# Performance work log

Measured on AMD Instinct MI355X. Metric: run time of the kernel, lower is better.

Reference implementation:

```python
import jax, jax.numpy as jnp
import numpy as np

DIM = 512
NUM_HEADS = 8
HEAD_DIM = DIM // NUM_HEADS
SCALE = HEAD_DIM ** -0.5


def setup_inputs() -> dict:
    key = jax.random.key(0)
    kx, kqw, kqb, kpw, kpb = jax.random.split(key, 5)
    B, N = 2, 4096
    x = jax.random.normal(kx, (B, N, DIM), dtype=jnp.float32)
    # nn.Linear weights stored as [out, in]; init ~ U(-1/sqrt(in), 1/sqrt(in))
    bound = 1.0 / np.sqrt(DIM)
    qkv_w = jax.random.uniform(kqw, (3 * DIM, DIM), minval=-bound, maxval=bound, dtype=jnp.float32)
    qkv_b = jax.random.uniform(kqb, (3 * DIM,), minval=-bound, maxval=bound, dtype=jnp.float32)
    proj_w = jax.random.uniform(kpw, (DIM, DIM), minval=-bound, maxval=bound, dtype=jnp.float32)
    proj_b = jax.random.uniform(kpb, (DIM,), minval=-bound, maxval=bound, dtype=jnp.float32)
    return {"x": x, "qkv_w": qkv_w, "qkv_b": qkv_b, "proj_w": proj_w, "proj_b": proj_b}


def reference(x, qkv_w, qkv_b, proj_w, proj_b):
    B, N, C = x.shape
    # qkv: [B, N, 3C] -> [3, B, H, N, Dh]
    qkv = x @ qkv_w.T + qkv_b
    qkv = qkv.reshape(B, N, 3, NUM_HEADS, HEAD_DIM).transpose(2, 0, 3, 1, 4)
    q, k, v = qkv[0], qkv[1], qkv[2]
    # scores: [B, H, N, N] (materialized, matching the original math)
    attn = jnp.einsum("bhqd,bhkd->bhqk", q, k) * SCALE
    attn = jax.nn.softmax(attn, axis=-1)
    out = jnp.einsum("bhqk,bhkd->bhqd", attn, v)  # [B, H, N, Dh]
    out = out.transpose(0, 2, 1, 3).reshape(B, N, C)
    return out @ proj_w.T + proj_b
```

## Files before the change

kernel.cpp:

```cpp
#include <hip/hip_runtime.h>
#include <stdint.h>
#include <stddef.h>

typedef __attribute__((ext_vector_type(8))) short short8;
typedef __attribute__((ext_vector_type(4))) float f32x4;

#define MFMA16(a, b, c) __builtin_amdgcn_mfma_f32_16x16x32_bf16((a), (b), (c), 0, 0, 0)

__device__ __forceinline__ float b2f(short x) {
    unsigned u = ((unsigned)(unsigned short)x) << 16;
    float f; __builtin_memcpy(&f, &u, 4); return f;
}
__device__ __forceinline__ short f2b(float f) {
    unsigned u; __builtin_memcpy(&u, &f, 4);
    u = (u + 0x7FFFu + ((u >> 16) & 1u)) >> 16;
    return (short)u;
}
__device__ __forceinline__ unsigned pack2(float a, float b) {
    unsigned ua, ub; __builtin_memcpy(&ua, &a, 4); __builtin_memcpy(&ub, &b, 4);
    return __builtin_amdgcn_perm(ub + 0x8000u, ua + 0x8000u, 0x07060302u);
}
__device__ __forceinline__ short8 load8f(const float* p) {
    const float4 f0 = *(const float4*)p;
    const float4 f1 = *(const float4*)(p + 4);
    short8 r;
    r[0]=f2b(f0.x); r[1]=f2b(f0.y); r[2]=f2b(f0.z); r[3]=f2b(f0.w);
    r[4]=f2b(f1.x); r[5]=f2b(f1.y); r[6]=f2b(f1.z); r[7]=f2b(f1.w);
    return r;
}

__global__ __launch_bounds__(256) void cvt3(
    const float* __restrict__ s0, short* __restrict__ d0, int n0,
    const float* __restrict__ s1, short* __restrict__ d1, int n1,
    const float* __restrict__ s2, short* __restrict__ d2, int n2)
{
    int i = blockIdx.x * 256 + threadIdx.x;
    if (i < n0) { *(short8*)(d0 + (size_t)i * 8) = load8f(s0 + (size_t)i * 8); return; }
    i -= n0;
    if (i < n1) { *(short8*)(d1 + (size_t)i * 8) = load8f(s1 + (size_t)i * 8); return; }
    i -= n1;
    if (i < n2) { *(short8*)(d2 + (size_t)i * 8) = load8f(s2 + (size_t)i * 8); }
}

__global__ __launch_bounds__(256) void qkv_qk(
    const short* __restrict__ X, const short* __restrict__ W,
    const float* __restrict__ bias,
    short* __restrict__ Qb, short* __restrict__ Kb)
{
    const int tid  = threadIdx.x;
    const int wv   = tid >> 6;
    const int lane = tid & 63;
    const int l15  = lane & 15;
    const int quad = lane >> 4;
    const int m0   = blockIdx.x * 128 + (wv >> 1) * 64;
    const int sec  = blockIdx.y >> 2;
    const int bis  = blockIdx.y & 3;
    const int nbase = sec * 512 + bis * 128;
    const int j0   = (wv & 1) * 64;

    const f32x4 zero = {0.f, 0.f, 0.f, 0.f};
    f32x4 acc[4][4];
#pragma unroll
    for (int i = 0; i < 4; i++)
#pragma unroll
        for (int j = 0; j < 4; j++) acc[i][j] = zero;

    for (int k0 = 0; k0 < 512; k0 += 32) {
        short8 a[4], b[4];
#pragma unroll
        for (int i = 0; i < 4; i++)
            a[i] = *(const short8*)(X + (size_t)(m0 + i * 16 + l15) * 512 + k0 + quad * 8);
#pragma unroll
        for (int j = 0; j < 4; j++)
            b[j] = *(const short8*)(W + (size_t)(nbase + j0 + j * 16 + l15) * 512 + k0 + quad * 8);
#pragma unroll
        for (int i = 0; i < 4; i++)
#pragma unroll
            for (int j = 0; j < 4; j++)
                acc[i][j] = MFMA16(a[i], b[j], acc[i][j]);
    }

#pragma unroll
    for (int j = 0; j < 4; j++) {
        const int jc = bis * 128 + j0 + j * 16 + l15;
        const float bs = bias[sec * 512 + jc];
        const int hl = jc >> 6, d = jc & 63;
#pragma unroll
        for (int i = 0; i < 4; i++) {
#pragma unroll
            for (int r = 0; r < 4; r++) {
                const int m = m0 + i * 16 + quad * 4 + r;
                const int bb = m >> 12, seq = m & 4095;
                const int bh = bb * 8 + hl;
                const float v = acc[i][j][r] + bs;
                if (sec == 0)
                    Qb[((size_t)bh * 4096 + seq) * 64 + d] = f2b(v * 0.125f);
                else
                    Kb[((size_t)bh * 4096 + seq) * 64 + d] = f2b(v);
            }
        }
    }
}

__global__ __launch_bounds__(256) void qkv_v(
    const short* __restrict__ X, const short* __restrict__ W,
    const float* __restrict__ bias, short* __restrict__ Vb)
{
    __shared__ short sT[128][132];

    const int tid  = threadIdx.x;
    const int wv   = tid >> 6;
    const int lane = tid & 63;
    const int l15  = lane & 15;
    const int quad = lane >> 4;
    const int m0   = blockIdx.x * 128 + (wv >> 1) * 64;
    const int bis  = blockIdx.y;
    const int nbase = 1024 + bis * 128;
    const int j0   = (wv & 1) * 64;

    const f32x4 zero = {0.f, 0.f, 0.f, 0.f};
    f32x4 acc[4][4];
#pragma unroll
    for (int i = 0; i < 4; i++)
#pragma unroll
        for (int j = 0; j < 4; j++) acc[i][j] = zero;

    for (int k0 = 0; k0 < 512; k0 += 32) {
        short8 a[4], b[4];
#pragma unroll
        for (int i = 0; i < 4; i++)
            a[i] = *(const short8*)(X + (size_t)(m0 + i * 16 + l15) * 512 + k0 + quad * 8);
#pragma unroll
        for (int j = 0; j < 4; j++)
            b[j] = *(const short8*)(W + (size_t)(nbase + j0 + j * 16 + l15) * 512 + k0 + quad * 8);
#pragma unroll
        for (int i = 0; i < 4; i++)
#pragma unroll
            for (int j = 0; j < 4; j++)
                acc[i][j] = MFMA16(a[i], b[j], acc[i][j]);
    }

#pragma unroll
    for (int j = 0; j < 4; j++) {
        const int jcl = j0 + j * 16 + l15;
        const float bs = bias[nbase + jcl];
#pragma unroll
        for (int i = 0; i < 4; i++) {
            uint2 w;
            w.x = pack2(acc[i][j][0] + bs, acc[i][j][1] + bs);
            w.y = pack2(acc[i][j][2] + bs, acc[i][j][3] + bs);
            *(uint2*)&sT[jcl][(wv >> 1) * 64 + i * 16 + quad * 4] = w;
        }
    }
    __syncthreads();

    const int jcl = tid >> 1, half = tid & 1;
    const int hl = (bis * 128 + jcl) >> 6;
    const int d  = jcl & 63;
    const int bb = (blockIdx.x * 128) >> 12;
    const int seq0 = ((blockIdx.x * 128) & 4095) + half * 64;
    short* dst = Vb + ((size_t)(bb * 8 + hl) * 64 + d) * 4096 + seq0;
#pragma unroll
    for (int u = 0; u < 8; u++)
        *(short8*)(dst + u * 8) = *(const short8*)&sT[jcl][half * 64 + u * 8];
}

__global__ __launch_bounds__(256) void flash_attn(
    const short* __restrict__ Q, const short* __restrict__ K,
    const short* __restrict__ V, short* __restrict__ PO0,
    short* __restrict__ PO1, float* __restrict__ lbuf, int ktiles)
{
    __shared__ short sK[64][72];
    __shared__ short sV[64][72];
    __shared__ short sP[4][2][16][72];

    const int tid  = threadIdx.x;
    const int wv   = tid >> 6;
    const int lane = tid & 63;
    const int l15  = lane & 15;
    const int quad = lane >> 4;
    const int bh = blockIdx.y;
    const int b = bh >> 3, h = bh & 7;
    const int qw = blockIdx.x * 128 + wv * 32;
    const int ks = blockIdx.z;
    const int key0 = ks * ktiles * 64;

    const short* Qb = Q + (size_t)bh * 4096 * 64;
    const short* Kb = K + (size_t)bh * 4096 * 64;
    const short* Vb = V + (size_t)bh * 64 * 4096;

    const short8 aq00 = *(const short8*)(Qb + (size_t)(qw + l15) * 64 + quad * 8);
    const short8 aq01 = *(const short8*)(Qb + (size_t)(qw + l15) * 64 + 32 + quad * 8);
    const short8 aq10 = *(const short8*)(Qb + (size_t)(qw + 16 + l15) * 64 + quad * 8);
    const short8 aq11 = *(const short8*)(Qb + (size_t)(qw + 16 + l15) * 64 + 32 + quad * 8);

    const f32x4 zero = {0.f, 0.f, 0.f, 0.f};
    f32x4 o0[4], o1[4];
    float l0 = 0.f, l1 = 0.f;
#pragma unroll
    for (int r = 0; r < 4; r++) { o0[r] = zero; o1[r] = zero; }

    int srow[2], scb[2];
#pragma unroll
    for (int i = 0; i < 2; i++) {
        const int c = tid + i * 256;
        srow[i] = c >> 3; scb[i] = (c & 7) * 8;
    }

    short8 pk[2], pv[2];
#pragma unroll
    for (int i = 0; i < 2; i++) {
        pk[i] = *(const short8*)(Kb + (size_t)(key0 + srow[i]) * 64 + scb[i]);
        pv[i] = *(const short8*)(Vb + (size_t)srow[i] * 4096 + key0 + scb[i]);
    }

    for (int kt = 0; kt < ktiles; ++kt) {
        const int k0 = key0 + kt * 64;
        __syncthreads();
#pragma unroll
        for (int i = 0; i < 2; i++) {
            *(short8*)&sK[srow[i]][scb[i]] = pk[i];
            *(short8*)&sV[srow[i]][scb[i]] = pv[i];
        }
        __syncthreads();

        if (kt + 1 < ktiles) {
            const int k0n = k0 + 64;
#pragma unroll
            for (int i = 0; i < 2; i++) {
                pk[i] = *(const short8*)(Kb + (size_t)(k0n + srow[i]) * 64 + scb[i]);
                pv[i] = *(const short8*)(Vb + (size_t)srow[i] * 4096 + k0n + scb[i]);
            }
        }

        f32x4 ST0[4], ST1[4];
#pragma unroll
        for (int c = 0; c < 4; c++) {
            const short8 bk0 = *(const short8*)&sK[c * 16 + l15][quad * 8];
            const short8 bk1 = *(const short8*)&sK[c * 16 + l15][32 + quad * 8];
            ST0[c] = MFMA16(bk1, aq01, MFMA16(bk0, aq00, zero));
            ST1[c] = MFMA16(bk1, aq11, MFMA16(bk0, aq10, zero));
        }

#pragma unroll
        for (int c = 0; c < 4; c++) {
            const float p0 = __expf(ST0[c][0]), p1 = __expf(ST0[c][1]);
            const float p2 = __expf(ST0[c][2]), p3 = __expf(ST0[c][3]);
            l0 += (p0 + p1) + (p2 + p3);
            uint2 w; w.x = pack2(p0, p1); w.y = pack2(p2, p3);
            *(uint2*)&sP[wv][0][l15][c * 16 + quad * 4] = w;
            const float r0 = __expf(ST1[c][0]), r1 = __expf(ST1[c][1]);
            const float r2 = __expf(ST1[c][2]), r3 = __expf(ST1[c][3]);
            l1 += (r0 + r1) + (r2 + r3);
            uint2 v; v.x = pack2(r0, r1); v.y = pack2(r2, r3);
            *(uint2*)&sP[wv][1][l15][c * 16 + quad * 4] = v;
        }
        __threadfence_block();

        const short8 bp00 = *(const short8*)&sP[wv][0][l15][quad * 8];
        const short8 bp01 = *(const short8*)&sP[wv][0][l15][32 + quad * 8];
        const short8 bp10 = *(const short8*)&sP[wv][1][l15][quad * 8];
        const short8 bp11 = *(const short8*)&sP[wv][1][l15][32 + quad * 8];

#pragma unroll
        for (int td = 0; td < 4; td++) {
            const short8 bv0 = *(const short8*)&sV[td * 16 + l15][quad * 8];
            const short8 bv1 = *(const short8*)&sV[td * 16 + l15][32 + quad * 8];
            o0[td] = MFMA16(bv0, bp00, o0[td]);
            o0[td] = MFMA16(bv1, bp01, o0[td]);
            o1[td] = MFMA16(bv0, bp10, o1[td]);
            o1[td] = MFMA16(bv1, bp11, o1[td]);
        }
    }

    l0 += __shfl_xor(l0, 16); l0 += __shfl_xor(l0, 32);
    l1 += __shfl_xor(l1, 16); l1 += __shfl_xor(l1, 32);
    const float inv0 = 1.f / fmaxf(l0, 1e-30f);
    const float inv1 = 1.f / fmaxf(l1, 1e-30f);

    short* PO = (ks == 0) ? PO0 : PO1;
#pragma unroll
    for (int td = 0; td < 4; td++) {
        uint2 w0, w1;
        w0.x = pack2(o0[td][0] * inv0, o0[td][1] * inv0);
        w0.y = pack2(o0[td][2] * inv0, o0[td][3] * inv0);
        w1.x = pack2(o1[td][0] * inv1, o1[td][1] * inv1);
        w1.y = pack2(o1[td][2] * inv1, o1[td][3] * inv1);
        const int col = h * 64 + td * 16 + quad * 4;
        *(uint2*)(PO + ((size_t)b * 4096 + qw + l15) * 512 + col) = w0;
        *(uint2*)(PO + ((size_t)b * 4096 + qw + 16 + l15) * 512 + col) = w1;
    }
    if (lbuf && quad == 0) {
        lbuf[((size_t)ks * 16 + bh) * 4096 + qw + l15] = l0;
        lbuf[((size_t)ks * 16 + bh) * 4096 + qw + 16 + l15] = l1;
    }
}

__global__ __launch_bounds__(256) void combine(
    const short* __restrict__ PO0, short* __restrict__ PO1,
    const float* __restrict__ L)
{
    const int i = blockIdx.x * 256 + threadIdx.x;
    const size_t flat = (size_t)i * 8;
    const int col = (int)(flat & 511);
    const int q   = (int)((flat >> 9) & 4095);
    const int b   = (int)(flat >> 21);
    const int bh  = b * 8 + (col >> 6);
    const float l0 = L[(size_t)bh * 4096 + q];
    const float l1 = L[(size_t)65536 + (size_t)bh * 4096 + q];
    const float inv = 1.f / (l0 + l1);
    const float w0 = l0 * inv, w1 = l1 * inv;
    const short8 a = *(const short8*)(PO0 + flat);
    const short8 c = *(const short8*)(PO1 + flat);
    short8 r;
#pragma unroll
    for (int k = 0; k < 8; k++) r[k] = f2b(w0 * b2f(a[k]) + w1 * b2f(c[k]));
    *(short8*)(PO1 + flat) = r;
}

__global__ __launch_bounds__(256) void proj_piece(
    const short* __restrict__ A, const short* __restrict__ W,
    const float* __restrict__ bias, float* __restrict__ dst, int m_base)
{
    const int tid  = threadIdx.x;
    const int wv   = tid >> 6;
    const int lane = tid & 63;
    const int l15  = lane & 15;
    const int quad = lane >> 4;
    const int m0 = blockIdx.x * 128 + (wv >> 1) * 64;
    const int n0 = blockIdx.y * 128 + (wv & 1) * 64;

    const f32x4 zero = {0.f, 0.f, 0.f, 0.f};
    f32x4 acc[4][4];
#pragma unroll
    for (int i = 0; i < 4; i++)
#pragma unroll
        for (int j = 0; j < 4; j++) acc[i][j] = zero;

    for (int k0 = 0; k0 < 512; k0 += 32) {
        short8 a[4], b[4];
#pragma unroll
        for (int i = 0; i < 4; i++)
            a[i] = *(const short8*)(A + (size_t)(m_base + m0 + i * 16 + l15) * 512 + k0 + quad * 8);
#pragma unroll
        for (int j = 0; j < 4; j++)
            b[j] = *(const short8*)(W + (size_t)(n0 + j * 16 + l15) * 512 + k0 + quad * 8);
#pragma unroll
        for (int i = 0; i < 4; i++)
#pragma unroll
            for (int j = 0; j < 4; j++)
                acc[i][j] = MFMA16(a[i], b[j], acc[i][j]);
    }

#pragma unroll
    for (int j = 0; j < 4; j++) {
        const int n = n0 + j * 16 + l15;
        const float bs = bias[n];
#pragma unroll
        for (int i = 0; i < 4; i++) {
#pragma unroll
            for (int r = 0; r < 4; r++) {
                const int m = m0 + i * 16 + quad * 4 + r;
                dst[(size_t)m * 512 + n] = acc[i][j][r] + bs;
            }
        }
    }
}

extern "C" void kernel_launch(void* const* d_in, const int* in_sizes, int n_in,
                              void* d_out, int out_size, void* d_ws, size_t ws_size,
                              hipStream_t stream)
{
    const float* x      = (const float*)d_in[0];
    const float* qkv_w  = (const float*)d_in[1];
    const float* qkv_b  = (const float*)d_in[2];
    const float* proj_w = (const float*)d_in[3];
    const float* proj_b = (const float*)d_in[4];

    const size_t MB = 1024 * 1024;
    short* xb   = (short*)d_out;
    short* wb   = (short*)d_out + 4 * MB;
    short* attn = (short*)d_out + 4 * MB;
    float* out  = (float*)d_out;

    short* Qf = (short*)d_ws;
    short* Kf = Qf + (size_t)16 * 4096 * 64;
    short* Vf = Kf + (size_t)16 * 4096 * 64;
    float* lbuf = (float*)((char*)d_ws + 24 * MB);
    short* pwb  = (short*)((char*)d_ws + 24 * MB + 512 * 1024);

    cvt3<<<2560, 256, 0, stream>>>(x, xb, 524288, qkv_w, wb, 98304, proj_w, pwb, 32768);
    qkv_qk<<<dim3(64, 8), 256, 0, stream>>>(xb, wb, qkv_b, Qf, Kf);
    qkv_v <<<dim3(64, 4), 256, 0, stream>>>(xb, wb, qkv_b, Vf);
    flash_attn<<<dim3(32, 16, 2), 256, 0, stream>>>(Qf, Kf, Vf, (short*)d_out, attn, lbuf, 32);
    combine<<<2048, 256, 0, stream>>>((const short*)d_out, attn, lbuf);
    proj_piece<<<dim3(32, 4), 256, 0, stream>>>(attn, pwb, proj_b, out, 0);
    proj_piece<<<dim3(32, 4), 256, 0, stream>>>(attn, pwb, proj_b, (float*)d_ws, 4096);
    hipMemcpyAsync((char*)d_out + 8 * MB, d_ws, 8 * MB,
                   hipMemcpyDeviceToDevice, stream);
}
```

Measured before the change: 281.7 us.

## Merge QKV GEMMs, compute softmax row sums via MFMA, use exp2 and hardware bf16 packing

```diff
diff --git a/kernel.cpp b/kernel.cpp
--- a/kernel.cpp
+++ b/kernel.cpp
@@ -1,4 +1,5 @@
 #include <hip/hip_runtime.h>
+#include <hip/hip_bf16.h>
 #include <stdint.h>
 #include <stddef.h>
 
@@ -6,6 +7,8 @@
 typedef __attribute__((ext_vector_type(4))) float f32x4;
 
 #define MFMA16(a, b, c) __builtin_amdgcn_mfma_f32_16x16x32_bf16((a), (b), (c), 0, 0, 0)
+
+#define QSCALE 0.1803368801111204f
 
 __device__ __forceinline__ float b2f(short x) {
     unsigned u = ((unsigned)(unsigned short)x) << 16;
@@ -16,9 +19,9 @@
     u = (u + 0x7FFFu + ((u >> 16) & 1u)) >> 16;
     return (short)u;
 }
-__device__ __forceinline__ unsigned pack2(float a, float b) {
-    unsigned ua, ub; __builtin_memcpy(&ua, &a, 4); __builtin_memcpy(&ub, &b, 4);
-    return __builtin_amdgcn_perm(ub + 0x8000u, ua + 0x8000u, 0x07060302u);
+__device__ __forceinline__ unsigned pkrn(float a, float b) {
+    __hip_bfloat162 h = __float22bfloat162_rn(float2{a, b});
+    unsigned u; __builtin_memcpy(&u, &h, 4); return u;
 }
 __device__ __forceinline__ short8 load8f(const float* p) {
     const float4 f0 = *(const float4*)p;
@@ -42,11 +45,13 @@
     if (i < n2) { *(short8*)(d2 + (size_t)i * 8) = load8f(s2 + (size_t)i * 8); }
 }
 
-__global__ __launch_bounds__(256) void qkv_qk(
+__global__ __launch_bounds__(256) void qkv_gemm(
     const short* __restrict__ X, const short* __restrict__ W,
     const float* __restrict__ bias,
-    short* __restrict__ Qb, short* __restrict__ Kb)
-{
+    short* __restrict__ Qb, short* __restrict__ Kb, short* __restrict__ Vb)
+{
+    __shared__ short sT[128][132];
+
     const int tid  = threadIdx.x;
     const int wv   = tid >> 6;
     const int lane = tid & 63;
@@ -80,89 +85,50 @@
                 acc[i][j] = MFMA16(a[i], b[j], acc[i][j]);
     }
 
-#pragma unroll
-    for (int j = 0; j < 4; j++) {
-        const int jc = bis * 128 + j0 + j * 16 + l15;
-        const float bs = bias[sec * 512 + jc];
-        const int hl = jc >> 6, d = jc & 63;
-#pragma unroll
-        for (int i = 0; i < 4; i++) {
-#pragma unroll
-            for (int r = 0; r < 4; r++) {
-                const int m = m0 + i * 16 + quad * 4 + r;
-                const int bb = m >> 12, seq = m & 4095;
-                const int bh = bb * 8 + hl;
-                const float v = acc[i][j][r] + bs;
-                if (sec == 0)
-                    Qb[((size_t)bh * 4096 + seq) * 64 + d] = f2b(v * 0.125f);
-                else
-                    Kb[((size_t)bh * 4096 + seq) * 64 + d] = f2b(v);
+    if (sec < 2) {
+        const float scale = (sec == 0) ? QSCALE : 1.0f;
+        short* dst = (sec == 0) ? Qb : Kb;
+#pragma unroll
+        for (int j = 0; j < 4; j++) {
+            const int jc = bis * 128 + j0 + j * 16 + l15;
+            const float bs = bias[sec * 512 + jc];
+            const int hl = jc >> 6, d = jc & 63;
+#pragma unroll
+            for (int i = 0; i < 4; i++) {
+#pragma unroll
+                for (int r = 0; r < 4; r++) {
+                    const int m = m0 + i * 16 + quad * 4 + r;
+                    const int bb = m >> 12, seq = m & 4095;
+                    dst[((size_t)(bb * 8 + hl) * 4096 + seq) * 64 + d] =
+                        f2b((acc[i][j][r] + bs) * scale);
+                }
             }
         }
-    }
-}
-
-__global__ __launch_bounds__(256) void qkv_v(
-    const short* __restrict__ X, const short* __restrict__ W,
-    const float* __restrict__ bias, short* __restrict__ Vb)
-{
-    __shared__ short sT[128][132];
-
-    const int tid  = threadIdx.x;
-    const int wv   = tid >> 6;
-    const int lane = tid & 63;
-    const int l15  = lane & 15;
-    const int quad = lane >> 4;
-    const int m0   = blockIdx.x * 128 + (wv >> 1) * 64;
-    const int bis  = blockIdx.y;
-    const int nbase = 1024 + bis * 128;
-    const int j0   = (wv & 1) * 64;
-
-    const f32x4 zero = {0.f, 0.f, 0.f, 0.f};
-    f32x4 acc[4][4];
-#pragma unroll
-    for (int i = 0; i < 4; i++)
-#pragma unroll
-        for (int j = 0; j < 4; j++) acc[i][j] = zero;
-
-    for (int k0 = 0; k0 < 512; k0 += 32) {
-        short8 a[4], b[4];
-#pragma unroll
-        for (int i = 0; i < 4; i++)
-            a[i] = *(const short8*)(X + (size_t)(m0 + i * 16 + l15) * 512 + k0 + quad * 8);
-#pragma unroll
-        for (int j = 0; j < 4; j++)
-            b[j] = *(const short8*)(W + (size_t)(nbase + j0 + j * 16 + l15) * 512 + k0 + quad * 8);
-#pragma unroll
-        for (int i = 0; i < 4; i++)
-#pragma unroll
-            for (int j = 0; j < 4; j++)
-                acc[i][j] = MFMA16(a[i], b[j], acc[i][j]);
-    }
-
-#pragma unroll
-    for (int j = 0; j < 4; j++) {
-        const int jcl = j0 + j * 16 + l15;
-        const float bs = bias[nbase + jcl];
-#pragma unroll
-        for (int i = 0; i < 4; i++) {
-            uint2 w;
-            w.x = pack2(acc[i][j][0] + bs, acc[i][j][1] + bs);
-            w.y = pack2(acc[i][j][2] + bs, acc[i][j][3] + bs);
-            *(uint2*)&sT[jcl][(wv >> 1) * 64 + i * 16 + quad * 4] = w;
-        }
-    }
-    __syncthreads();
-
-    const int jcl = tid >> 1, half = tid & 1;
-    const int hl = (bis * 128 + jcl) >> 6;
-    const int d  = jcl & 63;
-    const int bb = (blockIdx.x * 128) >> 12;
-    const int seq0 = ((blockIdx.x * 128) & 4095) + half * 64;
-    short* dst = Vb + ((size_t)(bb * 8 + hl) * 64 + d) * 4096 + seq0;
-#pragma unroll
-    for (int u = 0; u < 8; u++)
-        *(short8*)(dst + u * 8) = *(const short8*)&sT[jcl][half * 64 + u * 8];
+    } else {
+#pragma unroll
+        for (int j = 0; j < 4; j++) {
+            const int jcl = j0 + j * 16 + l15;
+            const float bs = bias[nbase + jcl];
+#pragma unroll
+            for (int i = 0; i < 4; i++) {
+                uint2 w;
+                w.x = pkrn(acc[i][j][0] + bs, acc[i][j][1] + bs);
+                w.y = pkrn(acc[i][j][2] + bs, acc[i][j][3] + bs);
+                *(uint2*)&sT[jcl][(wv >> 1) * 64 + i * 16 + quad * 4] = w;
+            }
+        }
+        __syncthreads();
+
+        const int jcl = tid >> 1, half = tid & 1;
+        const int hl = (bis * 128 + jcl) >> 6;
+        const int d  = jcl & 63;
+        const int bb = (blockIdx.x * 128) >> 12;
+        const int seq0 = ((blockIdx.x * 128) & 4095) + half * 64;
+        short* dst = Vb + ((size_t)(bb * 8 + hl) * 64 + d) * 4096 + seq0;
+#pragma unroll
+        for (int u = 0; u < 8; u++)
+            *(short8*)(dst + u * 8) = *(const short8*)&sT[jcl][half * 64 + u * 8];
+    }
 }
 
 __global__ __launch_bounds__(256) void flash_attn(
@@ -196,9 +162,12 @@
 
     const f32x4 zero = {0.f, 0.f, 0.f, 0.f};
     f32x4 o0[4], o1[4];
-    float l0 = 0.f, l1 = 0.f;
+    f32x4 lac0 = zero, lac1 = zero;
 #pragma unroll
     for (int r = 0; r < 4; r++) { o0[r] = zero; o1[r] = zero; }
+    const short one_bf = (short)0x3F80;
+    const short8 ones = {one_bf, one_bf, one_bf, one_bf,
+                         one_bf, one_bf, one_bf, one_bf};
 
     int srow[2], scb[2];
 #pragma unroll
@@ -206,7 +175,6 @@
         const int c = tid + i * 256;
         srow[i] = c >> 3; scb[i] = (c & 7) * 8;
     }
-
     short8 pk[2], pv[2];
 #pragma unroll
     for (int i = 0; i < 2; i++) {
@@ -244,15 +212,13 @@
 
 #pragma unroll
         for (int c = 0; c < 4; c++) {
-            const float p0 = __expf(ST0[c][0]), p1 = __expf(ST0[c][1]);
-            const float p2 = __expf(ST0[c][2]), p3 = __expf(ST0[c][3]);
-            l0 += (p0 + p1) + (p2 + p3);
-            uint2 w; w.x = pack2(p0, p1); w.y = pack2(p2, p3);
+            uint2 w;
+            w.x = pkrn(exp2f(ST0[c][0]), exp2f(ST0[c][1]));
+            w.y = pkrn(exp2f(ST0[c][2]), exp2f(ST0[c][3]));
             *(uint2*)&sP[wv][0][l15][c * 16 + quad * 4] = w;
-            const float r0 = __expf(ST1[c][0]), r1 = __expf(ST1[c][1]);
-            const float r2 = __expf(ST1[c][2]), r3 = __expf(ST1[c][3]);
-            l1 += (r0 + r1) + (r2 + r3);
-            uint2 v; v.x = pack2(r0, r1); v.y = pack2(r2, r3);
+            uint2 v;
+            v.x = pkrn(exp2f(ST1[c][0]), exp2f(ST1[c][1]));
+            v.y = pkrn(exp2f(ST1[c][2]), exp2f(ST1[c][3]));
             *(uint2*)&sP[wv][1][l15][c * 16 + quad * 4] = v;
         }
         __threadfence_block();
@@ -261,6 +227,11 @@
         const short8 bp01 = *(const short8*)&sP[wv][0][l15][32 + quad * 8];
         const short8 bp10 = *(const short8*)&sP[wv][1][l15][quad * 8];
         const short8 bp11 = *(const short8*)&sP[wv][1][l15][32 + quad * 8];
+
+        lac0 = MFMA16(ones, bp00, lac0);
+        lac0 = MFMA16(ones, bp01, lac0);
+        lac1 = MFMA16(ones, bp10, lac1);
+        lac1 = MFMA16(ones, bp11, lac1);
 
 #pragma unroll
         for (int td = 0; td < 4; td++) {
@@ -273,8 +244,8 @@
         }
     }
 
-    l0 += __shfl_xor(l0, 16); l0 += __shfl_xor(l0, 32);
-    l1 += __shfl_xor(l1, 16); l1 += __shfl_xor(l1, 32);
+    const float l0 = lac0[0];
+    const float l1 = lac1[0];
     const float inv0 = 1.f / fmaxf(l0, 1e-30f);
     const float inv1 = 1.f / fmaxf(l1, 1e-30f);
 
@@ -282,15 +253,15 @@
 #pragma unroll
     for (int td = 0; td < 4; td++) {
         uint2 w0, w1;
-        w0.x = pack2(o0[td][0] * inv0, o0[td][1] * inv0);
-        w0.y = pack2(o0[td][2] * inv0, o0[td][3] * inv0);
-        w1.x = pack2(o1[td][0] * inv1, o1[td][1] * inv1);
-        w1.y = pack2(o1[td][2] * inv1, o1[td][3] * inv1);
+        w0.x = pkrn(o0[td][0] * inv0, o0[td][1] * inv0);
+        w0.y = pkrn(o0[td][2] * inv0, o0[td][3] * inv0);
+        w1.x = pkrn(o1[td][0] * inv1, o1[td][1] * inv1);
+        w1.y = pkrn(o1[td][2] * inv1, o1[td][3] * inv1);
         const int col = h * 64 + td * 16 + quad * 4;
         *(uint2*)(PO + ((size_t)b * 4096 + qw + l15) * 512 + col) = w0;
         *(uint2*)(PO + ((size_t)b * 4096 + qw + 16 + l15) * 512 + col) = w1;
     }
-    if (lbuf && quad == 0) {
+    if (quad == 0) {
         lbuf[((size_t)ks * 16 + bh) * 4096 + qw + l15] = l0;
         lbuf[((size_t)ks * 16 + bh) * 4096 + qw + 16 + l15] = l1;
     }
@@ -314,7 +285,12 @@
     const short8 c = *(const short8*)(PO1 + flat);
     short8 r;
 #pragma unroll
-    for (int k = 0; k < 8; k++) r[k] = f2b(w0 * b2f(a[k]) + w1 * b2f(c[k]));
+    for (int k = 0; k < 8; k += 2) {
+        const unsigned p = pkrn(w0 * b2f(a[k]) + w1 * b2f(c[k]),
+                                w0 * b2f(a[k + 1]) + w1 * b2f(c[k + 1]));
+        r[k]     = (short)(p & 0xFFFF);
+        r[k + 1] = (short)(p >> 16);
+    }
     *(short8*)(PO1 + flat) = r;
 }
 
@@ -380,7 +356,9 @@
     const size_t MB = 1024 * 1024;
     short* xb   = (short*)d_out;
     short* wb   = (short*)d_out + 4 * MB;
-    short* attn = (short*)d_out + 4 * MB;
+    short* PO0  = (short*)d_out;
+    short* PO1  = (short*)d_out + 4 * MB;
+    short* attn = PO1;
     float* out  = (float*)d_out;
 
     short* Qf = (short*)d_ws;
@@ -390,10 +368,9 @@
     short* pwb  = (short*)((char*)d_ws + 24 * MB + 512 * 1024);
 
     cvt3<<<2560, 256, 0, stream>>>(x, xb, 524288, qkv_w, wb, 98304, proj_w, pwb, 32768);
-    qkv_qk<<<dim3(64, 8), 256, 0, stream>>>(xb, wb, qkv_b, Qf, Kf);
-    qkv_v <<<dim3(64, 4), 256, 0, stream>>>(xb, wb, qkv_b, Vf);
-    flash_attn<<<dim3(32, 16, 2), 256, 0, stream>>>(Qf, Kf, Vf, (short*)d_out, attn, lbuf, 32);
-    combine<<<2048, 256, 0, stream>>>((const short*)d_out, attn, lbuf);
+    qkv_gemm<<<dim3(64, 12), 256, 0, stream>>>(xb, wb, qkv_b, Qf, Kf, Vf);
+    flash_attn<<<dim3(32, 16, 2), 256, 0, stream>>>(Qf, Kf, Vf, PO0, PO1, lbuf, 32);
+    combine<<<2048, 256, 0, stream>>>((const short*)PO0, attn, lbuf);
     proj_piece<<<dim3(32, 4), 256, 0, stream>>>(attn, pwb, proj_b, out, 0);
     proj_piece<<<dim3(32, 4), 256, 0, stream>>>(attn, pwb, proj_b, (float*)d_ws, 4096);
     hipMemcpyAsync((char*)d_out + 8 * MB, d_ws, 8 * MB,
```

After: 296.1 us. 1.05x slower.
